# Kernel optimization log

Measured on AMD Instinct MI355X. Metric: run time of the kernel, lower is better.

The kernel has to match this reference:

```python
import jax, jax.numpy as jnp
import numpy as np

N = 50000
E = 500000
D_IN = 128
D_HID = 128  # hidden_channels; conv1 outputs 2*D_HID


def setup_inputs() -> dict:
    key = jax.random.key(0)
    ks = jax.random.split(key, 8)
    x = jax.random.normal(ks[0], (N, D_IN), dtype=jnp.float32)
    edge_index = jax.random.randint(ks[1], (2, E), 0, N, dtype=jnp.int64)
    # Glorot-ish init for weights, zeros for biases (PyG GCNConv default style)
    W1 = jax.random.normal(ks[2], (D_IN, 2 * D_HID), dtype=jnp.float32) / np.sqrt(D_IN)
    b1 = jnp.zeros((2 * D_HID,), dtype=jnp.float32)
    W2 = jax.random.normal(ks[3], (2 * D_HID, D_HID), dtype=jnp.float32) / np.sqrt(2 * D_HID)
    b2 = jnp.zeros((D_HID,), dtype=jnp.float32)
    Wfc = jax.random.normal(ks[4], (D_HID, 6), dtype=jnp.float32) / np.sqrt(D_HID)
    bfc = jnp.zeros((6,), dtype=jnp.float32)
    return {"x": x, "W1": W1, "b1": b1, "W2": W2, "b2": b2,
            "Wfc": Wfc, "bfc": bfc, "edge_index": edge_index}


def _gcn_conv(x, W, b, src, dst, deg_isqrt, n):
    # PyG GCNConv: h = W x; out_i = sum_j norm_ij * h_j + b, with self-loops
    h = x @ W                                  # [n, d_out]
    norm = deg_isqrt[src] * deg_isqrt[dst]     # [E+n]
    msg = h[src] * norm[:, None]               # gather + scale
    out = jax.ops.segment_sum(msg, dst, num_segments=n)  # scatter-add
    return out + b


def reference(x, W1, b1, W2, b2, Wfc, bfc, edge_index):
    n = x.shape[0]
    loop = jnp.arange(n, dtype=edge_index.dtype)
    src = jnp.concatenate([edge_index[0], loop])  # add self-loops
    dst = jnp.concatenate([edge_index[1], loop])
    deg = jax.ops.segment_sum(jnp.ones_like(dst, dtype=x.dtype), dst, num_segments=n)
    deg_isqrt = jnp.where(deg > 0, jax.lax.rsqrt(jnp.maximum(deg, 1e-12)), 0.0)
    h = jax.nn.relu(_gcn_conv(x, W1, b1, src, dst, deg_isqrt, n))
    h = jax.nn.relu(_gcn_conv(h, W2, b2, src, dst, deg_isqrt, n))
    return h @ Wfc + bfc
```

## Files before the change

### kernel.cpp

```cpp
#include <hip/hip_runtime.h>


typedef _Float16 f16;
typedef __attribute__((ext_vector_type(8))) _Float16 f16x8;
typedef __attribute__((ext_vector_type(4))) float f32x4;

__global__ void count_kernel(const int* __restrict__ dst, int* __restrict__ cnt,
                             int e) {
    for (int i = blockIdx.x * blockDim.x + threadIdx.x; i < e;
         i += gridDim.x * blockDim.x)
        atomicAdd(&cnt[dst[i]], 1);
}

__global__ void disq_kernel(const int* __restrict__ cnt, float* __restrict__ disq,
                            int n) {
    int i = blockIdx.x * blockDim.x + threadIdx.x;
    if (i < n) disq[i] = rsqrtf(1.0f + (float)cnt[i]);
}

__global__ void scan1_kernel(const int* __restrict__ cnt, int* __restrict__ local,
                             int* __restrict__ partials, int n) {
    __shared__ int lds[256];
    int base = blockIdx.x * 1024;
    int t = threadIdx.x;
    int v[4];
    int sum = 0;
    #pragma unroll
    for (int j = 0; j < 4; j++) {
        int i = base + t * 4 + j;
        v[j] = (i < n) ? cnt[i] : 0;
        sum += v[j];
    }
    lds[t] = sum;
    __syncthreads();
    for (int off = 1; off < 256; off <<= 1) {
        int x = (t >= off) ? lds[t - off] : 0;
        __syncthreads();
        lds[t] += x;
        __syncthreads();
    }
    int excl = lds[t] - sum;
    if (t == 255) partials[blockIdx.x] = lds[255];
    int run = excl;
    #pragma unroll
    for (int j = 0; j < 4; j++) {
        int i = base + t * 4 + j;
        if (i < n) local[i] = run;
        run += v[j];
    }
}

__global__ void scan2_kernel(int* __restrict__ partials, int nb) {
    __shared__ int lds[1024];
    int t = threadIdx.x;
    int v = (t < nb) ? partials[t] : 0;
    lds[t] = v;
    __syncthreads();
    for (int off = 1; off < 1024; off <<= 1) {
        int x = (t >= off) ? lds[t - off] : 0;
        __syncthreads();
        lds[t] += x;
        __syncthreads();
    }
    if (t < nb) partials[t] = lds[t] - v;
}

__global__ void scan3_kernel(const int* __restrict__ local,
                             const int* __restrict__ partials,
                             int* __restrict__ row_ptr, int* __restrict__ cursor,
                             int n, int e_total) {
    int base = blockIdx.x * 1024;
    int add = partials[blockIdx.x];
    int t = threadIdx.x;
    #pragma unroll
    for (int j = 0; j < 4; j++) {
        int i = base + t * 4 + j;
        if (i < n) {
            int p = local[i] + add;
            row_ptr[i] = p;
            cursor[i] = p;
        }
    }
    if (blockIdx.x == 0 && t == 0) row_ptr[n] = e_total;
}

__global__ void csr_fill_kernel(const int* __restrict__ src, const int* __restrict__ dst,
                                int* __restrict__ cursor, int* __restrict__ esorted,
                                int e) {
    for (int i = blockIdx.x * blockDim.x + threadIdx.x; i < e;
         i += gridDim.x * blockDim.x) {
        int d = dst[i];
        int pos = atomicAdd(&cursor[d], 1);
        esorted[pos] = src[i];
    }
}

__global__ void cvt_f32_f16_kernel(const float4* __restrict__ in,
                                   f16* __restrict__ out, long long n4) {
    long long i = blockIdx.x * (long long)blockDim.x + threadIdx.x;
    if (i >= n4) return;
    float4 v = in[i];
    union { f16 h[4]; short4 s; } u;
    u.h[0] = (f16)v.x; u.h[1] = (f16)v.y; u.h[2] = (f16)v.z; u.h[3] = (f16)v.w;
    *(short4*)(out + i * 4) = u.s;
}

__global__ void cvt_wt_kernel(const float* __restrict__ W, f16* __restrict__ Wt,
                              int K, int Nc) {
    int i = blockIdx.x * blockDim.x + threadIdx.x;
    if (i >= K * Nc) return;
    int n = i / K, k = i - n * K;
    Wt[i] = (f16)W[(long long)k * Nc + n];
}

__global__ __launch_bounds__(256)
void gemm_f16_kernel(const f16* __restrict__ A,
                     const f16* __restrict__ Bt,
                     f16* __restrict__ C,
                     const float* __restrict__ rowscale,
                     int M, int K, int Nc) {
    __shared__ __align__(16) char smem[(128 * 64 + 64 * 64) * 2];
    char* As = smem;
    char* Bs = smem + 128 * 64 * 2;
    const int tid = threadIdx.x;
    const int lane = tid & 63;
    const int wid = tid >> 6;
    const int wr = wid >> 1;
    const int wc = wid & 1;
    const int row0 = blockIdx.y * 128;
    const int col0 = blockIdx.x * 64;

    f32x4 acc[4][2];
    #pragma unroll
    for (int mr = 0; mr < 4; mr++)
        #pragma unroll
        for (int nr = 0; nr < 2; nr++)
            acc[mr][nr] = (f32x4){0.f, 0.f, 0.f, 0.f};

    for (int k0 = 0; k0 < K; k0 += 64) {
        #pragma unroll
        for (int i = 0; i < 4; i++) {
            int flat = tid + i * 256;
            int r = flat >> 3, g = flat & 7;
            int gr = row0 + r;
            float4 v = {0.f, 0.f, 0.f, 0.f};
            if (gr < M) v = *(const float4*)(A + (long long)gr * K + k0 + g * 8);
            *(float4*)(As + r * 128 + ((g * 16) ^ ((r & 7) << 4))) = v;
        }
        #pragma unroll
        for (int i = 0; i < 2; i++) {
            int flat = tid + i * 256;
            int nn = flat >> 3, g = flat & 7;
            float4 v = *(const float4*)(Bt + (long long)(col0 + nn) * K + k0 + g * 8);
            *(float4*)(Bs + nn * 128 + ((g * 16) ^ ((nn & 7) << 4))) = v;
        }
        __syncthreads();
        #pragma unroll
        for (int ks = 0; ks < 2; ks++) {
            const int kb = (ks * 32 + ((lane >> 4) * 8)) * 2;
            f16x8 af[4], bf[2];
            #pragma unroll
            for (int mr = 0; mr < 4; mr++) {
                int r = wr * 64 + mr * 16 + (lane & 15);
                af[mr] = *(const f16x8*)(As + r * 128 + (kb ^ ((r & 7) << 4)));
            }
            #pragma unroll
            for (int nr = 0; nr < 2; nr++) {
                int c = wc * 32 + nr * 16 + (lane & 15);
                bf[nr] = *(const f16x8*)(Bs + c * 128 + (kb ^ ((c & 7) << 4)));
            }
            #pragma unroll
            for (int mr = 0; mr < 4; mr++)
                #pragma unroll
                for (int nr = 0; nr < 2; nr++)
                    acc[mr][nr] = __builtin_amdgcn_mfma_f32_16x16x32_f16(
                        af[mr], bf[nr], acc[mr][nr], 0, 0, 0);
        }
        __syncthreads();
    }
    #pragma unroll
    for (int mr = 0; mr < 4; mr++) {
        #pragma unroll
        for (int reg = 0; reg < 4; reg++) {
            int row = row0 + wr * 64 + mr * 16 + (lane >> 4) * 4 + reg;
            if (row < M) {
                float s = rowscale[row];
                int col = col0 + wc * 32 + (lane & 15);
                #pragma unroll
                for (int nr = 0; nr < 2; nr++)
                    C[(long long)row * Nc + col + nr * 16] =
                        (f16)(acc[mr][nr][reg] * s);
            }
        }
    }
}

__global__ void gather_relu_f16_kernel(const float4* __restrict__ h,
                                       float4* __restrict__ out,
                                       const int* __restrict__ row_ptr,
                                       const int* __restrict__ esorted,
                                       const float* __restrict__ disq,
                                       const float* __restrict__ bias,
                                       int n, int c8) {
    int lane = threadIdx.x & 63;
    long long wave = (blockIdx.x * (long long)blockDim.x + threadIdx.x) >> 6;
    int epw = 64 / c8;
    int sub = lane / c8;
    int sl = lane - sub * c8;
    long long node = wave * epw + sub;
    if (node >= n) return;
    int beg = row_ptr[node], end = row_ptr[node + 1];
    float acc[8];
    {
        float4 v = h[node * c8 + sl];
        const f16* hp = (const f16*)&v;
        #pragma unroll
        for (int j = 0; j < 8; j++) acc[j] = (float)hp[j];
    }
    for (int e = beg; e < end; e++) {
        int s = esorted[e];
        float4 v = h[(long long)s * c8 + sl];
        const f16* hp = (const f16*)&v;
        #pragma unroll
        for (int j = 0; j < 8; j++) acc[j] += (float)hp[j];
    }
    float sc = disq[node];
    const float4* b4 = (const float4*)(bias + sl * 8);
    float4 b0 = b4[0], b1 = b4[1];
    float bb[8] = {b0.x, b0.y, b0.z, b0.w, b1.x, b1.y, b1.z, b1.w};
    union { float4 f4; f16 hh[8]; } o;
    #pragma unroll
    for (int j = 0; j < 8; j++)
        o.hh[j] = (f16)fmaxf(fmaf(acc[j], sc, bb[j]), 0.0f);
    out[node * c8 + sl] = o.f4;
}

__global__ void final_fc_kernel(const f16* __restrict__ h,
                                const float* __restrict__ Wfc,
                                const float* __restrict__ bfc,
                                float* __restrict__ out, int n) {
    __shared__ float wf[128 * 6];
    for (int i = threadIdx.x; i < 128 * 6; i += blockDim.x) wf[i] = Wfc[i];
    __syncthreads();
    int lane = threadIdx.x & 63;
    int wave = (blockIdx.x * blockDim.x + threadIdx.x) >> 6;
    int nwaves = (gridDim.x * blockDim.x) >> 6;
    for (int node = wave; node < n; node += nwaves) {
        const f16* hp = h + (long long)node * 128 + lane * 2;
        float v0 = (float)hp[0], v1 = (float)hp[1];
        float acc[6];
        #pragma unroll
        for (int j = 0; j < 6; j++)
            acc[j] = v0 * wf[(2 * lane) * 6 + j] + v1 * wf[(2 * lane + 1) * 6 + j];
        #pragma unroll
        for (int off = 32; off >= 1; off >>= 1)
            #pragma unroll
            for (int j = 0; j < 6; j++) acc[j] += __shfl_down(acc[j], off);
        if (lane == 0) {
            #pragma unroll
            for (int j = 0; j < 6; j++)
                out[(long long)node * 6 + j] = acc[j] + bfc[j];
        }
    }
}

extern "C" void kernel_launch(void* const* d_in, const int* in_sizes, int n_in,
                              void* d_out, int out_size, void* d_ws, size_t ws_size,
                              hipStream_t stream) {
    const float* x   = (const float*)d_in[0];
    const float* W1  = (const float*)d_in[1];
    const float* b1  = (const float*)d_in[2];
    const float* W2  = (const float*)d_in[3];
    const float* b2  = (const float*)d_in[4];
    const float* Wfc = (const float*)d_in[5];
    const float* bfc = (const float*)d_in[6];
    const int* edges = (const int*)d_in[7];

    const int N = in_sizes[0] / 128;
    const int E = in_sizes[7] / 2;
    const int* e_src = edges;
    const int* e_dst = edges + E;

    char* ws = (char*)d_ws;
    size_t off = 0;
    auto alloc = [&](size_t bytes) {
        void* p = ws + off;
        off += (bytes + 255) & ~(size_t)255;
        return p;
    };
    const int NB = (N + 1023) / 1024;
    float* disq     = (float*)alloc((size_t)N * 4);
    int*   cnt      = (int*)  alloc((size_t)N * 4);
    int*   slocal   = (int*)  alloc((size_t)N * 4);
    int*   partials = (int*)  alloc((size_t)NB * 4);
    int*   row_ptr  = (int*)  alloc((size_t)(N + 1) * 4);
    int*   cursor   = (int*)  alloc((size_t)N * 4);
    int*   esorted  = (int*)  alloc((size_t)E * 4);
    f16*   x_h      = (f16*)  alloc((size_t)N * 128 * 2);
    f16*   wt1      = (f16*)  alloc((size_t)256 * 128 * 2);
    f16*   wt2      = (f16*)  alloc((size_t)128 * 256 * 2);
    f16*   hbuf     = (f16*)  alloc((size_t)N * 256 * 2);
    f16*   gbuf     = (f16*)  alloc((size_t)N * 256 * 2);
    (void)ws_size; (void)n_in;

    float* out = (float*)d_out; (void)out_size;

    hipMemsetAsync(cnt, 0, (size_t)N * sizeof(int), stream);
    count_kernel<<<2048, 256, 0, stream>>>(e_dst, cnt, E);
    disq_kernel<<<(N + 255) / 256, 256, 0, stream>>>(cnt, disq, N);
    scan1_kernel<<<NB, 256, 0, stream>>>(cnt, slocal, partials, N);
    scan2_kernel<<<1, 1024, 0, stream>>>(partials, NB);
    scan3_kernel<<<NB, 256, 0, stream>>>(slocal, partials, row_ptr, cursor, N, E);
    csr_fill_kernel<<<2048, 256, 0, stream>>>(e_src, e_dst, cursor, esorted, E);

    {
        long long n4 = (long long)N * 128 / 4;
        cvt_f32_f16_kernel<<<(int)((n4 + 255) / 256), 256, 0, stream>>>(
            (const float4*)x, x_h, n4);
    }
    cvt_wt_kernel<<<(128 * 256 + 255) / 256, 256, 0, stream>>>(W1, wt1, 128, 256);
    cvt_wt_kernel<<<(256 * 128 + 255) / 256, 256, 0, stream>>>(W2, wt2, 256, 128);

    {
        dim3 g(256 / 64, (N + 127) / 128);
        gemm_f16_kernel<<<g, 256, 0, stream>>>(x_h, wt1, hbuf, disq, N, 128, 256);
    }
    {
        long long waves = ((long long)N + 1) / 2;
        int blocks = (int)((waves + 3) / 4);
        gather_relu_f16_kernel<<<blocks, 256, 0, stream>>>(
            (const float4*)hbuf, (float4*)gbuf, row_ptr, esorted, disq, b1, N, 32);
    }

    {
        dim3 g(128 / 64, (N + 127) / 128);
        gemm_f16_kernel<<<g, 256, 0, stream>>>(gbuf, wt2, hbuf, disq, N, 256, 128);
    }
    {
        long long waves = ((long long)N + 3) / 4;
        int blocks = (int)((waves + 3) / 4);
        gather_relu_f16_kernel<<<blocks, 256, 0, stream>>>(
            (const float4*)hbuf, (float4*)gbuf, row_ptr, esorted, disq, b2, N, 16);
    }

    final_fc_kernel<<<1024, 256, 0, stream>>>(gbuf, Wfc, bfc, out, N);
}
```

Measured before the change: 279.8 us.

## Aggregate before first GEMM and fuse bias/ReLU into GEMM, FC into gather

Reorders layer 1 so the sparse neighbour aggregation runs on the 128-wide pre-scaled input instead of the 256-wide GEMM output, halving gather traffic for that layer. Bias, normalisation and ReLU for layer 1 move into the GEMM epilogue. Layer 2's gather is fused with bias, ReLU and the final 128x6 FC projection, removing one full pass over the hidden buffer. The degree-normalisation kernel is folded into the scan. Pre-scaling x before f16 conversion slightly changes rounding.

```diff
diff --git a/kernel.cpp b/kernel.cpp
--- a/kernel.cpp
+++ b/kernel.cpp
@@ -12,14 +12,9 @@
         atomicAdd(&cnt[dst[i]], 1);
 }
 
-__global__ void disq_kernel(const int* __restrict__ cnt, float* __restrict__ disq,
-                            int n) {
-    int i = blockIdx.x * blockDim.x + threadIdx.x;
-    if (i < n) disq[i] = rsqrtf(1.0f + (float)cnt[i]);
-}
-
 __global__ void scan1_kernel(const int* __restrict__ cnt, int* __restrict__ local,
-                             int* __restrict__ partials, int n) {
+                             int* __restrict__ partials, float* __restrict__ disq,
+                             int n) {
     __shared__ int lds[256];
     int base = blockIdx.x * 1024;
     int t = threadIdx.x;
@@ -29,6 +24,7 @@
     for (int j = 0; j < 4; j++) {
         int i = base + t * 4 + j;
         v[j] = (i < n) ? cnt[i] : 0;
+        if (i < n) disq[i] = rsqrtf(1.0f + (float)v[j]);
         sum += v[j];
     }
     lds[t] = sum;
@@ -95,14 +91,17 @@
     }
 }
 
-__global__ void cvt_f32_f16_kernel(const float4* __restrict__ in,
-                                   f16* __restrict__ out, long long n4) {
+__global__ void scale_cvt_kernel(const float4* __restrict__ in,
+                                 const float* __restrict__ disq,
+                                 f16* __restrict__ out, long long n4) {
     long long i = blockIdx.x * (long long)blockDim.x + threadIdx.x;
     if (i >= n4) return;
     float4 v = in[i];
-    union { f16 h[4]; short4 s; } u;
-    u.h[0] = (f16)v.x; u.h[1] = (f16)v.y; u.h[2] = (f16)v.z; u.h[3] = (f16)v.w;
-    *(short4*)(out + i * 4) = u.s;
+    float s = disq[i >> 5];
+    union { f16 h[4]; short4 s4; } u;
+    u.h[0] = (f16)(v.x * s); u.h[1] = (f16)(v.y * s);
+    u.h[2] = (f16)(v.z * s); u.h[3] = (f16)(v.w * s);
+    *(short4*)(out + i * 4) = u.s4;
 }
 
 __global__ void cvt_wt_kernel(const float* __restrict__ W, f16* __restrict__ Wt,
@@ -113,11 +112,13 @@
     Wt[i] = (f16)W[(long long)k * Nc + n];
 }
 
+template <int MODE>
 __global__ __launch_bounds__(256)
 void gemm_f16_kernel(const f16* __restrict__ A,
                      const f16* __restrict__ Bt,
                      f16* __restrict__ C,
                      const float* __restrict__ rowscale,
+                     const float* __restrict__ bias,
                      int M, int K, int Nc) {
     __shared__ __align__(16) char smem[(128 * 64 + 64 * 64) * 2];
     char* As = smem;
@@ -178,6 +179,12 @@
         }
         __syncthreads();
     }
+    float bv[2] = {0.f, 0.f};
+    if (MODE == 1) {
+        #pragma unroll
+        for (int nr = 0; nr < 2; nr++)
+            bv[nr] = bias[col0 + wc * 32 + nr * 16 + (lane & 15)];
+    }
     #pragma unroll
     for (int mr = 0; mr < 4; mr++) {
         #pragma unroll
@@ -187,21 +194,21 @@
                 float s = rowscale[row];
                 int col = col0 + wc * 32 + (lane & 15);
                 #pragma unroll
-                for (int nr = 0; nr < 2; nr++)
-                    C[(long long)row * Nc + col + nr * 16] =
-                        (f16)(acc[mr][nr][reg] * s);
+                for (int nr = 0; nr < 2; nr++) {
+                    float v = acc[mr][nr][reg] * s;
+                    if (MODE == 1) v = fmaxf(v + bv[nr], 0.0f);
+                    C[(long long)row * Nc + col + nr * 16] = (f16)v;
+                }
             }
         }
     }
 }
 
-__global__ void gather_relu_f16_kernel(const float4* __restrict__ h,
-                                       float4* __restrict__ out,
-                                       const int* __restrict__ row_ptr,
-                                       const int* __restrict__ esorted,
-                                       const float* __restrict__ disq,
-                                       const float* __restrict__ bias,
-                                       int n, int c8) {
+__global__ void gather_sum_f16_kernel(const float4* __restrict__ h,
+                                      float4* __restrict__ out,
+                                      const int* __restrict__ row_ptr,
+                                      const int* __restrict__ esorted,
+                                      int n, int c8) {
     int lane = threadIdx.x & 63;
     long long wave = (blockIdx.x * (long long)blockDim.x + threadIdx.x) >> 6;
     int epw = 64 / c8;
@@ -224,43 +231,71 @@
         #pragma unroll
         for (int j = 0; j < 8; j++) acc[j] += (float)hp[j];
     }
-    float sc = disq[node];
-    const float4* b4 = (const float4*)(bias + sl * 8);
-    float4 b0 = b4[0], b1 = b4[1];
-    float bb[8] = {b0.x, b0.y, b0.z, b0.w, b1.x, b1.y, b1.z, b1.w};
     union { float4 f4; f16 hh[8]; } o;
     #pragma unroll
-    for (int j = 0; j < 8; j++)
-        o.hh[j] = (f16)fmaxf(fmaf(acc[j], sc, bb[j]), 0.0f);
+    for (int j = 0; j < 8; j++) o.hh[j] = (f16)acc[j];
     out[node * c8 + sl] = o.f4;
 }
 
-__global__ void final_fc_kernel(const f16* __restrict__ h,
-                                const float* __restrict__ Wfc,
-                                const float* __restrict__ bfc,
-                                float* __restrict__ out, int n) {
-    __shared__ float wf[128 * 6];
-    for (int i = threadIdx.x; i < 128 * 6; i += blockDim.x) wf[i] = Wfc[i];
+__global__ void gather_fc_kernel(const float4* __restrict__ t,
+                                 const int* __restrict__ row_ptr,
+                                 const int* __restrict__ esorted,
+                                 const float* __restrict__ disq,
+                                 const float* __restrict__ b2,
+                                 const float* __restrict__ Wfc,
+                                 const float* __restrict__ bfc,
+                                 float* __restrict__ out, int n) {
+    __shared__ float wf[6 * 132];
+    for (int i = threadIdx.x; i < 6 * 128; i += 256) {
+        int k = i >> 7, ch = i & 127;
+        wf[k * 132 + ch] = Wfc[ch * 6 + k];
+    }
     __syncthreads();
     int lane = threadIdx.x & 63;
-    int wave = (blockIdx.x * blockDim.x + threadIdx.x) >> 6;
-    int nwaves = (gridDim.x * blockDim.x) >> 6;
-    for (int node = wave; node < n; node += nwaves) {
-        const f16* hp = h + (long long)node * 128 + lane * 2;
-        float v0 = (float)hp[0], v1 = (float)hp[1];
-        float acc[6];
-        #pragma unroll
-        for (int j = 0; j < 6; j++)
-            acc[j] = v0 * wf[(2 * lane) * 6 + j] + v1 * wf[(2 * lane + 1) * 6 + j];
-        #pragma unroll
-        for (int off = 32; off >= 1; off >>= 1)
-            #pragma unroll
-            for (int j = 0; j < 6; j++) acc[j] += __shfl_down(acc[j], off);
-        if (lane == 0) {
-            #pragma unroll
-            for (int j = 0; j < 6; j++)
-                out[(long long)node * 6 + j] = acc[j] + bfc[j];
-        }
+    long long wave = (blockIdx.x * (long long)blockDim.x + threadIdx.x) >> 6;
+    int sub = lane >> 4;
+    int sl = lane & 15;
+    long long node = wave * 4 + sub;
+    if (node >= n) return;
+    int beg = row_ptr[node], end = row_ptr[node + 1];
+    float acc[8];
+    {
+        float4 v = t[node * 16 + sl];
+        const f16* hp = (const f16*)&v;
+        #pragma unroll
+        for (int j = 0; j < 8; j++) acc[j] = (float)hp[j];
+    }
+    for (int e = beg; e < end; e++) {
+        int s = esorted[e];
+        float4 v = t[(long long)s * 16 + sl];
+        const f16* hp = (const f16*)&v;
+        #pragma unroll
+        for (int j = 0; j < 8; j++) acc[j] += (float)hp[j];
+    }
+    float sc = disq[node];
+    const float4* b4 = (const float4*)(b2 + sl * 8);
+    float4 bb0 = b4[0], bb1 = b4[1];
+    float bb[8] = {bb0.x, bb0.y, bb0.z, bb0.w, bb1.x, bb1.y, bb1.z, bb1.w};
+    float h2[8];
+    #pragma unroll
+    for (int j = 0; j < 8; j++)
+        h2[j] = fmaxf(fmaf(acc[j], sc, bb[j]), 0.0f);
+    float p[6];
+    #pragma unroll
+    for (int k = 0; k < 6; k++) {
+        float s = 0.f;
+        #pragma unroll
+        for (int j = 0; j < 8; j++) s += h2[j] * wf[k * 132 + sl * 8 + j];
+        p[k] = s;
+    }
+    #pragma unroll
+    for (int off = 8; off >= 1; off >>= 1)
+        #pragma unroll
+        for (int k = 0; k < 6; k++) p[k] += __shfl_down(p[k], off);
+    if (sl == 0) {
+        #pragma unroll
+        for (int k = 0; k < 6; k++)
+            out[(long long)node * 6 + k] = p[k] + bfc[k];
     }
 }
 
@@ -296,52 +331,52 @@
     int*   row_ptr  = (int*)  alloc((size_t)(N + 1) * 4);
     int*   cursor   = (int*)  alloc((size_t)N * 4);
     int*   esorted  = (int*)  alloc((size_t)E * 4);
-    f16*   x_h      = (f16*)  alloc((size_t)N * 128 * 2);
+    f16*   xs       = (f16*)  alloc((size_t)N * 128 * 2);
     f16*   wt1      = (f16*)  alloc((size_t)256 * 128 * 2);
     f16*   wt2      = (f16*)  alloc((size_t)128 * 256 * 2);
-    f16*   hbuf     = (f16*)  alloc((size_t)N * 256 * 2);
-    f16*   gbuf     = (f16*)  alloc((size_t)N * 256 * 2);
+    f16*   agg1     = (f16*)  alloc((size_t)N * 128 * 2);
+    f16*   h1       = (f16*)  alloc((size_t)N * 256 * 2);
+    f16*   tbuf     = (f16*)  alloc((size_t)N * 128 * 2);
     (void)ws_size; (void)n_in;
 
     float* out = (float*)d_out; (void)out_size;
 
     hipMemsetAsync(cnt, 0, (size_t)N * sizeof(int), stream);
     count_kernel<<<2048, 256, 0, stream>>>(e_dst, cnt, E);
-    disq_kernel<<<(N + 255) / 256, 256, 0, stream>>>(cnt, disq, N);
-    scan1_kernel<<<NB, 256, 0, stream>>>(cnt, slocal, partials, N);
+    scan1_kernel<<<NB, 256, 0, stream>>>(cnt, slocal, partials, disq, N);
     scan2_kernel<<<1, 1024, 0, stream>>>(partials, NB);
     scan3_kernel<<<NB, 256, 0, stream>>>(slocal, partials, row_ptr, cursor, N, E);
     csr_fill_kernel<<<2048, 256, 0, stream>>>(e_src, e_dst, cursor, esorted, E);
 
     {
         long long n4 = (long long)N * 128 / 4;
-        cvt_f32_f16_kernel<<<(int)((n4 + 255) / 256), 256, 0, stream>>>(
-            (const float4*)x, x_h, n4);
+        scale_cvt_kernel<<<(int)((n4 + 255) / 256), 256, 0, stream>>>(
+            (const float4*)x, disq, xs, n4);
     }
     cvt_wt_kernel<<<(128 * 256 + 255) / 256, 256, 0, stream>>>(W1, wt1, 128, 256);
     cvt_wt_kernel<<<(256 * 128 + 255) / 256, 256, 0, stream>>>(W2, wt2, 256, 128);
 
     {
-        dim3 g(256 / 64, (N + 127) / 128);
-        gemm_f16_kernel<<<g, 256, 0, stream>>>(x_h, wt1, hbuf, disq, N, 128, 256);
-    }
-    {
-        long long waves = ((long long)N + 1) / 2;
-        int blocks = (int)((waves + 3) / 4);
-        gather_relu_f16_kernel<<<blocks, 256, 0, stream>>>(
-            (const float4*)hbuf, (float4*)gbuf, row_ptr, esorted, disq, b1, N, 32);
-    }
-
-    {
-        dim3 g(128 / 64, (N + 127) / 128);
-        gemm_f16_kernel<<<g, 256, 0, stream>>>(gbuf, wt2, hbuf, disq, N, 256, 128);
-    }
-    {
         long long waves = ((long long)N + 3) / 4;
         int blocks = (int)((waves + 3) / 4);
-        gather_relu_f16_kernel<<<blocks, 256, 0, stream>>>(
-            (const float4*)hbuf, (float4*)gbuf, row_ptr, esorted, disq, b2, N, 16);
-    }
-
-    final_fc_kernel<<<1024, 256, 0, stream>>>(gbuf, Wfc, bfc, out, N);
-}
+        gather_sum_f16_kernel<<<blocks, 256, 0, stream>>>(
+            (const float4*)xs, (float4*)agg1, row_ptr, esorted, N, 16);
+    }
+    {
+        dim3 g(256 / 64, (N + 127) / 128);
+        gemm_f16_kernel<1><<<g, 256, 0, stream>>>(agg1, wt1, h1, disq, b1,
+                                                  N, 128, 256);
+    }
+
+    {
+        dim3 g(128 / 64, (N + 127) / 128);
+        gemm_f16_kernel<0><<<g, 256, 0, stream>>>(h1, wt2, tbuf, disq, nullptr,
+                                                  N, 256, 128);
+    }
+    {
+        long long waves = ((long long)N + 3) / 4;
+        int blocks = (int)((waves + 3) / 4);
+        gather_fc_kernel<<<blocks, 256, 0, stream>>>(
+            (const float4*)tbuf, row_ptr, esorted, disq, b2, Wfc, bfc, out, N);
+    }
+}
```

New measurement: 240.2 us. 14.2% less time.
